# Optimization experiments

Hardware: AMD Instinct MI355X
Metric: run time of the kernel (lower is better)

Reference implementation:

```python
import jax, jax.numpy as jnp
import numpy as np

N_NODES = 100000
EMB_DIM = 64
N_EDGES = 1200000
N_LAYERS = 3


def setup_inputs() -> dict:
    key = jax.random.key(0)
    k1, k2, k3 = jax.random.split(key, 3)
    embedding = jax.random.normal(k1, (N_NODES, EMB_DIM), dtype=jnp.float32)
    layer_weights = jnp.ones((N_LAYERS + 1,), dtype=jnp.float32) / (N_LAYERS + 1)
    edge_weight = jax.random.uniform(k2, (N_EDGES,), dtype=jnp.float32)
    edge_index = jax.random.randint(k3, (2, N_EDGES), 0, N_NODES, dtype=jnp.int64)
    return {"embedding": embedding, "layer_weights": layer_weights,
            "edge_weight": edge_weight, "edge_index": edge_index}


def reference(embedding, layer_weights, edge_weight, edge_index):
    # LightGCN inference (dropout off). Each LGConv applies gcn_norm
    # (no self loops) then scatter-adds norm * x[src] into dst.
    n = embedding.shape[0]
    row, col = edge_index[0], edge_index[1]  # source, target

    # gcn_norm: deg over target nodes, symmetric normalization
    deg = jax.ops.segment_sum(edge_weight, col, num_segments=n)
    dinv = jnp.where(deg > 0, jax.lax.rsqrt(deg), 0.0)
    norm = dinv[row] * edge_weight * dinv[col]  # [E]

    x = embedding
    outs = [x]
    for _ in range(N_LAYERS):
        msgs = norm[:, None] * x[row]                         # [E, D] gather
        x = jax.ops.segment_sum(msgs, col, num_segments=n)    # [N, D] scatter
        outs.append(x)

    w = jax.nn.softmax(layer_weights)                         # [L+1]
    comb = jnp.einsum('l,lnd->nd', w, jnp.stack(outs))        # weighted layer combine
    # F.normalize(dim=1), eps=1e-12
    nrm = jnp.maximum(jnp.linalg.norm(comb, axis=1, keepdims=True), 1e-12)
    return comb / nrm
```

## Files before the change

kernel.cpp:

```cpp
#include <hip/hip_runtime.h>

#define N_NODES 100000
#define EMB_DIM 64
#define N_EDGES 1200000

#define BSHIFT  7
#define BNODES  128
#define NBUCKET ((N_NODES + BNODES - 1) / BNODES)
#define CAP     2048
#define EPB     4096
#define NBLK_BIN ((N_EDGES + EPB - 1) / EPB)

#define DBINS 512
#define DNPB  1024
#define NBLK_DEG ((N_NODES + DNPB - 1) / DNPB)

#define WSCALE 32767.0f
#define WINV   (1.0f / 32767.0f)

typedef unsigned short ushort8v __attribute__((ext_vector_type(8)));

struct __align__(8) BinRec {
    unsigned meta;
    float    ew;
};

__device__ __forceinline__ unsigned short f2bf(float f) {
    unsigned u = __float_as_uint(f);
    u += 0x7FFFu + ((u >> 16) & 1u);
    return (unsigned short)(u >> 16);
}
__device__ __forceinline__ float bf2f(unsigned short h) {
    return __uint_as_float((unsigned)h << 16);
}

__global__ void init_kernel(int* __restrict__ bucket_cursor, int* __restrict__ dhist) {
    int t = threadIdx.x;
    if (t < NBUCKET) bucket_cursor[t] = t * CAP;
    if (t < DBINS)   dhist[t] = 0;
}

__global__ void bin_scatter(const int* __restrict__ row,
                            const int* __restrict__ col,
                            const float* __restrict__ ew,
                            int* __restrict__ bucket_cursor,
                            BinRec* __restrict__ binned) {
    __shared__ int hcnt[NBUCKET];
    __shared__ int hbase[NBUCKET];
    int tid = threadIdx.x;
    if (tid < NBUCKET) hcnt[tid] = 0;
    __syncthreads();
    int base = blockIdx.x * EPB;
    int end = base + EPB; if (end > N_EDGES) end = N_EDGES;
    for (int e = base + tid; e < end; e += 1024)
        atomicAdd(&hcnt[col[e] >> BSHIFT], 1);
    __syncthreads();
    if (tid < NBUCKET) {
        int c = hcnt[tid];
        hbase[tid] = c ? atomicAdd(&bucket_cursor[tid], c) : 0;
        hcnt[tid] = 0;
    }
    __syncthreads();
    for (int e = base + tid; e < end; e += 1024) {
        int c = col[e];
        int b = c >> BSHIFT;
        int rk = atomicAdd(&hcnt[b], 1);
        BinRec r;
        r.meta = (unsigned)row[e] | ((unsigned)(c & (BNODES - 1)) << 20);
        r.ew = ew[e];
        binned[hbase[b] + rk] = r;
    }
}

__global__ void bucket_scan(const int* __restrict__ cursor,
                            int* __restrict__ csr_base,
                            int* __restrict__ start) {
    __shared__ int ws[16];
    int t = threadIdx.x;
    int lane = t & 63, wid = t >> 6;
    int v = (t < NBUCKET) ? (cursor[t] - t * CAP) : 0;
    int inc = v;
    #pragma unroll
    for (int o = 1; o < 64; o <<= 1) {
        int u = __shfl_up(inc, o, 64);
        if (lane >= o) inc += u;
    }
    if (lane == 63) ws[wid] = inc;
    __syncthreads();
    int woff = 0;
    for (int w = 0; w < wid; ++w) woff += ws[w];
    if (t < NBUCKET) csr_base[t] = woff + inc - v;
    if (t == 0) start[N_NODES] = N_EDGES;
}

__global__ void bucket_build(const BinRec* __restrict__ binned,
                             const int* __restrict__ cursor,
                             const int* __restrict__ csr_base,
                             const float* __restrict__ emb,
                             float* __restrict__ dinv,
                             float* __restrict__ rdinv,
                             int* __restrict__ start,
                             unsigned* __restrict__ rec,
                             unsigned short* __restrict__ y0,
                             int* __restrict__ dhist) {
    __shared__ BinRec lbin[CAP];
    __shared__ int   cnt[BNODES];
    __shared__ float deg[BNODES];
    __shared__ int   cur[BNODES];
    __shared__ int   dh[DBINS];
    __shared__ int   wsum[2];
    int b = blockIdx.x;
    int tid = threadIdx.x;
    if (tid < BNODES) { cnt[tid] = 0; deg[tid] = 0.0f; }
    for (int i = tid; i < DBINS; i += 256) dh[i] = 0;
    __syncthreads();
    int s = b * CAP;
    int n = cursor[b] - s;
    for (int i = tid; i < n; i += 256) {
        BinRec r = binned[s + i];
        lbin[i] = r;
        int l = r.meta >> 20;
        atomicAdd(&cnt[l], 1);
        atomicAdd(&deg[l], r.ew);
    }
    __syncthreads();
    int lane = tid & 63, wid = tid >> 6;
    int v = (tid < BNODES) ? cnt[tid] : 0;
    int inc = v;
    #pragma unroll
    for (int o = 1; o < 64; o <<= 1) {
        int u = __shfl_up(inc, o, 64);
        if (lane >= o) inc += u;
    }
    if (tid < BNODES && lane == 63) wsum[wid] = inc;
    __syncthreads();
    if (tid < BNODES) {
        int excl = inc - v + ((wid == 1) ? wsum[0] : 0);
        int node = (b << BSHIFT) + tid;
        if (node < N_NODES) {
            int st = csr_base[b] + excl;
            start[node] = st;
            cur[tid] = st;
            float d = deg[tid];
            dinv[node]  = (d > 0.0f) ? rsqrtf(d) : 0.0f;
            rdinv[node] = (d > 0.0f) ? sqrtf(d)  : 0.0f;
            int dd = v; if (dd > DBINS - 1) dd = DBINS - 1;
            atomicAdd(&dh[dd], 1);
        } else {
            cur[tid] = 0;
        }
    }
    __syncthreads();
    for (int i = tid; i < n; i += 256) {
        BinRec r = lbin[i];
        int l = r.meta >> 20;
        int pos = atomicAdd(&cur[l], 1);
        unsigned wq = (unsigned)rintf(r.ew * WSCALE);
        rec[pos] = ((r.meta & 0xFFFFFu) << 15) | wq;
    }
    for (int i = tid; i < DBINS; i += 256)
        if (dh[i]) atomicAdd(&dhist[i], dh[i]);
    #pragma unroll
    for (int pass = 0; pass < 4; ++pass) {
        int g = (pass * 256 + tid) * 8;
        int l = g >> 6;
        int node = (b << BSHIFT) + l;
        if (node < N_NODES) {
            float d = deg[l];
            float dn = (d > 0.0f) ? rsqrtf(d) : 0.0f;
            size_t off = (((size_t)node) << 6) + (g & 63);
            float4 a = *(const float4*)(emb + off);
            float4 bb = *(const float4*)(emb + off + 4);
            uint4 o;
            o.x = (unsigned)f2bf(dn * a.x)  | ((unsigned)f2bf(dn * a.y)  << 16);
            o.y = (unsigned)f2bf(dn * a.z)  | ((unsigned)f2bf(dn * a.w)  << 16);
            o.z = (unsigned)f2bf(dn * bb.x) | ((unsigned)f2bf(dn * bb.y) << 16);
            o.w = (unsigned)f2bf(dn * bb.z) | ((unsigned)f2bf(dn * bb.w) << 16);
            *(uint4*)(y0 + off) = o;
        }
    }
}

__global__ void deg_scan(const int* __restrict__ dhist, int* __restrict__ dcursor) {
    __shared__ int ws[8];
    int t = threadIdx.x;
    int lane = t & 63, wid = t >> 6;
    int v = dhist[t];
    int inc = v;
    #pragma unroll
    for (int o = 1; o < 64; o <<= 1) {
        int u = __shfl_up(inc, o, 64);
        if (lane >= o) inc += u;
    }
    if (lane == 63) ws[wid] = inc;
    __syncthreads();
    int woff = 0;
    for (int w = 0; w < wid; ++w) woff += ws[w];
    dcursor[t] = woff + inc - v;
}

__global__ void deg_scatter(const int* __restrict__ start,
                            int* __restrict__ dcursor,
                            int* __restrict__ perm) {
    __shared__ int h[DBINS];
    __shared__ int hb[DBINS];
    int tid = threadIdx.x;
    for (int i = tid; i < DBINS; i += 256) h[i] = 0;
    __syncthreads();
    int base = blockIdx.x * DNPB;
    int end = base + DNPB; if (end > N_NODES) end = N_NODES;
    for (int n = base + tid; n < end; n += 256) {
        int d = start[n + 1] - start[n];
        if (d > DBINS - 1) d = DBINS - 1;
        atomicAdd(&h[d], 1);
    }
    __syncthreads();
    for (int i = tid; i < DBINS; i += 256) {
        int c = h[i];
        hb[i] = c ? atomicAdd(&dcursor[i], c) : 0;
        h[i] = 0;
    }
    __syncthreads();
    for (int n = base + tid; n < end; n += 256) {
        int d = start[n + 1] - start[n];
        if (d > DBINS - 1) d = DBINS - 1;
        int rk = atomicAdd(&h[d], 1);
        perm[hb[d] + rk] = n;
    }
}

__device__ __forceinline__ void gather4(const unsigned* __restrict__ rec, int j,
                                        const unsigned short* __restrict__ yin, int q,
                                        float& a0, float& a1, float& a2, float& a3,
                                        float& a4, float& a5, float& a6, float& a7) {
    unsigned v0 = rec[j], v1 = rec[j + 1], v2 = rec[j + 2], v3 = rec[j + 3];
    ushort8v h0 = *(const ushort8v*)(yin + (((size_t)(v0 >> 15)) << 6) + q);
    ushort8v h1 = *(const ushort8v*)(yin + (((size_t)(v1 >> 15)) << 6) + q);
    ushort8v h2 = *(const ushort8v*)(yin + (((size_t)(v2 >> 15)) << 6) + q);
    ushort8v h3 = *(const ushort8v*)(yin + (((size_t)(v3 >> 15)) << 6) + q);
    float w0 = (float)(v0 & 0x7FFFu) * WINV, w1 = (float)(v1 & 0x7FFFu) * WINV;
    float w2 = (float)(v2 & 0x7FFFu) * WINV, w3 = (float)(v3 & 0x7FFFu) * WINV;
    a0 += w0*bf2f(h0[0]) + w1*bf2f(h1[0]) + w2*bf2f(h2[0]) + w3*bf2f(h3[0]);
    a1 += w0*bf2f(h0[1]) + w1*bf2f(h1[1]) + w2*bf2f(h2[1]) + w3*bf2f(h3[1]);
    a2 += w0*bf2f(h0[2]) + w1*bf2f(h1[2]) + w2*bf2f(h2[2]) + w3*bf2f(h3[2]);
    a3 += w0*bf2f(h0[3]) + w1*bf2f(h1[3]) + w2*bf2f(h2[3]) + w3*bf2f(h3[3]);
    a4 += w0*bf2f(h0[4]) + w1*bf2f(h1[4]) + w2*bf2f(h2[4]) + w3*bf2f(h3[4]);
    a5 += w0*bf2f(h0[5]) + w1*bf2f(h1[5]) + w2*bf2f(h2[5]) + w3*bf2f(h3[5]);
    a6 += w0*bf2f(h0[6]) + w1*bf2f(h1[6]) + w2*bf2f(h2[6]) + w3*bf2f(h3[6]);
    a7 += w0*bf2f(h0[7]) + w1*bf2f(h1[7]) + w2*bf2f(h2[7]) + w3*bf2f(h3[7]);
}

__device__ __forceinline__ void gather1(const unsigned* __restrict__ rec, int j,
                                        const unsigned short* __restrict__ yin, int q,
                                        float& a0, float& a1, float& a2, float& a3,
                                        float& a4, float& a5, float& a6, float& a7) {
    unsigned v = rec[j];
    ushort8v h = *(const ushort8v*)(yin + (((size_t)(v >> 15)) << 6) + q);
    float w = (float)(v & 0x7FFFu) * WINV;
    a0 += w * bf2f(h[0]); a1 += w * bf2f(h[1]);
    a2 += w * bf2f(h[2]); a3 += w * bf2f(h[3]);
    a4 += w * bf2f(h[4]); a5 += w * bf2f(h[5]);
    a6 += w * bf2f(h[6]); a7 += w * bf2f(h[7]);
}

#define ACC8 a0, a1, a2, a3, a4, a5, a6, a7

#define MERGE_SUBS()                                         \
    a0 += __shfl_xor(a0, 8, 64); a1 += __shfl_xor(a1, 8, 64); \
    a2 += __shfl_xor(a2, 8, 64); a3 += __shfl_xor(a3, 8, 64); \
    a4 += __shfl_xor(a4, 8, 64); a5 += __shfl_xor(a5, 8, 64); \
    a6 += __shfl_xor(a6, 8, 64); a7 += __shfl_xor(a7, 8, 64);

__global__ void prop8s_kernel(const unsigned short* __restrict__ yin,
                              unsigned short* __restrict__ yout,
                              const unsigned* __restrict__ rec,
                              const int* __restrict__ start,
                              const float* __restrict__ dinv,
                              const int* __restrict__ perm) {
    int t = blockIdx.x * blockDim.x + threadIdx.x;
    int g = t >> 4;
    int lane16 = t & 15;
    int sub = lane16 >> 3;
    int q = (lane16 & 7) << 3;
    if (g >= N_NODES) return;
    int n = perm[g];
    int s = start[n], e = start[n + 1];
    int d = e - s;
    int half = (d + 1) >> 1;
    int j  = s + sub * half;
    int j1 = sub ? e : s + half;

    float a0 = 0.f, a1 = 0.f, a2 = 0.f, a3 = 0.f;
    float a4 = 0.f, a5 = 0.f, a6 = 0.f, a7 = 0.f;
    for (; j + 4 <= j1; j += 4) gather4(rec, j, yin, q, ACC8);
    for (; j < j1; ++j)         gather1(rec, j, yin, q, ACC8);

    MERGE_SUBS();

    if (sub == 0) {
        float dn = dinv[n];
        float dn2 = dn * dn;
        uint4 o;
        o.x = (unsigned)f2bf(dn2 * a0) | ((unsigned)f2bf(dn2 * a1) << 16);
        o.y = (unsigned)f2bf(dn2 * a2) | ((unsigned)f2bf(dn2 * a3) << 16);
        o.z = (unsigned)f2bf(dn2 * a4) | ((unsigned)f2bf(dn2 * a5) << 16);
        o.w = (unsigned)f2bf(dn2 * a6) | ((unsigned)f2bf(dn2 * a7) << 16);
        *(uint4*)(yout + (((size_t)n) << 6) + q) = o;
    }
}

__global__ void prop8s_combine_kernel(const unsigned short* __restrict__ yin,
                                      const unsigned short* __restrict__ y0h,
                                      const unsigned short* __restrict__ y1h,
                                      const float* __restrict__ emb,
                                      const unsigned* __restrict__ rec,
                                      const int* __restrict__ start,
                                      const float* __restrict__ dinv,
                                      const float* __restrict__ rdinv,
                                      const float* __restrict__ lw,
                                      const int* __restrict__ perm,
                                      float* __restrict__ out) {
    int t = blockIdx.x * blockDim.x + threadIdx.x;
    int g = t >> 4;
    int lane16 = t & 15;
    int sub = lane16 >> 3;
    int q = (lane16 & 7) << 3;
    if (g >= N_NODES) return;
    int n = perm[g];
    int s = start[n], e = start[n + 1];
    int d = e - s;
    int half = (d + 1) >> 1;
    int j  = s + sub * half;
    int j1 = sub ? e : s + half;

    float a0 = 0.f, a1 = 0.f, a2 = 0.f, a3 = 0.f;
    float a4 = 0.f, a5 = 0.f, a6 = 0.f, a7 = 0.f;
    for (; j + 4 <= j1; j += 4) gather4(rec, j, yin, q, ACC8);
    for (; j < j1; ++j)         gather1(rec, j, yin, q, ACC8);

    MERGE_SUBS();

    if (sub == 0) {
        float dn = dinv[n];
        float rn = rdinv[n];

        float w0 = lw[0], w1 = lw[1], w2 = lw[2], w3 = lw[3];
        float m = fmaxf(fmaxf(w0, w1), fmaxf(w2, w3));
        float e0 = expf(w0 - m), e1 = expf(w1 - m), e2 = expf(w2 - m), e3 = expf(w3 - m);
        float inv_s = 1.0f / (e0 + e1 + e2 + e3);
        float c0 = e0 * rn, c1 = e1 * rn, c2 = e2 * rn, c3 = e3 * dn;

        size_t off = (((size_t)n) << 6) + q;
        float v0, v1, v2, v3, v4, v5, v6, v7;
        if (rn != 0.0f) {
            ushort8v h0v = *(const ushort8v*)(y0h + off);
            ushort8v h1v = *(const ushort8v*)(y1h + off);
            ushort8v h2v = *(const ushort8v*)(yin + off);
            v0 = (c0 * bf2f(h0v[0]) + c1 * bf2f(h1v[0]) + c2 * bf2f(h2v[0]) + c3 * a0) * inv_s;
            v1 = (c0 * bf2f(h0v[1]) + c1 * bf2f(h1v[1]) + c2 * bf2f(h2v[1]) + c3 * a1) * inv_s;
            v2 = (c0 * bf2f(h0v[2]) + c1 * bf2f(h1v[2]) + c2 * bf2f(h2v[2]) + c3 * a2) * inv_s;
            v3 = (c0 * bf2f(h0v[3]) + c1 * bf2f(h1v[3]) + c2 * bf2f(h2v[3]) + c3 * a3) * inv_s;
            v4 = (c0 * bf2f(h0v[4]) + c1 * bf2f(h1v[4]) + c2 * bf2f(h2v[4]) + c3 * a4) * inv_s;
            v5 = (c0 * bf2f(h0v[5]) + c1 * bf2f(h1v[5]) + c2 * bf2f(h2v[5]) + c3 * a5) * inv_s;
            v6 = (c0 * bf2f(h0v[6]) + c1 * bf2f(h1v[6]) + c2 * bf2f(h2v[6]) + c3 * a6) * inv_s;
            v7 = (c0 * bf2f(h0v[7]) + c1 * bf2f(h1v[7]) + c2 * bf2f(h2v[7]) + c3 * a7) * inv_s;
        } else {
            float4 xa = *(const float4*)(emb + off);
            float4 xb = *(const float4*)(emb + off + 4);
            float c = e0 * inv_s;
            v0 = c * xa.x; v1 = c * xa.y; v2 = c * xa.z; v3 = c * xa.w;
            v4 = c * xb.x; v5 = c * xb.y; v6 = c * xb.z; v7 = c * xb.w;
        }

        float sq = v0*v0 + v1*v1 + v2*v2 + v3*v3 + v4*v4 + v5*v5 + v6*v6 + v7*v7;
        #pragma unroll
        for (int o = 1; o < 8; o <<= 1) sq += __shfl_xor(sq, o, 64);
        float nrm = fmaxf(sqrtf(sq), 1e-12f);
        float inv_n = 1.0f / nrm;

        float4 oa, ob;
        oa.x = v0 * inv_n; oa.y = v1 * inv_n; oa.z = v2 * inv_n; oa.w = v3 * inv_n;
        ob.x = v4 * inv_n; ob.y = v5 * inv_n; ob.z = v6 * inv_n; ob.w = v7 * inv_n;
        *(float4*)(out + off) = oa;
        *(float4*)(out + off + 4) = ob;
    }
}

extern "C" void kernel_launch(void* const* d_in, const int* in_sizes, int n_in,
                              void* d_out, int out_size, void* d_ws, size_t ws_size,
                              hipStream_t stream) {
    const float* emb = (const float*)d_in[0];
    const float* lw  = (const float*)d_in[1];
    const float* ew  = (const float*)d_in[2];
    const int*   ei  = (const int*)d_in[3];
    const int* row = ei;
    const int* col = ei + N_EDGES;
    float* out = (float*)d_out;

    char* p = (char*)d_ws;
    BinRec*  binned = (BinRec*)p;               p += (size_t)NBUCKET * CAP * sizeof(BinRec);
    unsigned* rec   = (unsigned*)p;             p += (size_t)N_EDGES * 4;
    unsigned short* y0h = (unsigned short*)p;   p += (size_t)N_NODES * EMB_DIM * 2;
    unsigned short* y1h = (unsigned short*)p;   p += (size_t)N_NODES * EMB_DIM * 2;
    unsigned short* y2h = (unsigned short*)p;   p += (size_t)N_NODES * EMB_DIM * 2;
    float* dinv  = (float*)p;                   p += (size_t)N_NODES * 4;
    float* rdinv = (float*)p;                   p += (size_t)N_NODES * 4;
    int*   startA= (int*)p;                     p += (size_t)(N_NODES + 8) * 4;
    int*   perm  = (int*)p;                     p += (size_t)N_NODES * 4;
    int*   csr_base      = (int*)p;             p += (size_t)NBUCKET * 4;
    int*   bucket_cursor = (int*)p;             p += (size_t)NBUCKET * 4;
    int*   dhist   = (int*)p;                   p += (size_t)DBINS * 4;
    int*   dcursor = (int*)p;                   p += (size_t)DBINS * 4;

    const int B = 256;

    init_kernel<<<1, 1024, 0, stream>>>(bucket_cursor, dhist);
    bin_scatter<<<NBLK_BIN, 1024, 0, stream>>>(row, col, ew, bucket_cursor, binned);
    bucket_scan<<<1, 1024, 0, stream>>>(bucket_cursor, csr_base, startA);
    bucket_build<<<NBUCKET, B, 0, stream>>>(binned, bucket_cursor, csr_base, emb,
                                            dinv, rdinv, startA, rec, y0h, dhist);
    deg_scan<<<1, DBINS, 0, stream>>>(dhist, dcursor);
    deg_scatter<<<NBLK_DEG, B, 0, stream>>>(startA, dcursor, perm);

    long pt = (long)N_NODES * 16;
    int pgrid = (int)((pt + B - 1) / B);
    prop8s_kernel<<<pgrid, B, 0, stream>>>(y0h, y1h, rec, startA, dinv, perm);
    prop8s_kernel<<<pgrid, B, 0, stream>>>(y1h, y2h, rec, startA, dinv, perm);
    prop8s_combine_kernel<<<pgrid, B, 0, stream>>>(y2h, y0h, y1h, emb, rec, startA,
                                                   dinv, rdinv, lw, perm, out);
}
```

Before: 152.4 us.

## Use 8 lanes per node with prefetched edge records and reversed degree order

The propagation kernels now give each node 8 threads instead of 16, so the two-way edge split and the shuffle merge go away. The gather loop loads the next four edge records in software before the current ones are processed. Nodes are visited in reverse degree-sorted order, so high-degree nodes start first. bin_scatter also stages column indices in shared memory so they are not re-read from global memory. The trade-off is half the parallelism per node, which lengthens the serial chains for high-degree nodes, plus extra shared memory use in the binning kernel.

```diff
diff --git a/kernel.cpp b/kernel.cpp
--- a/kernel.cpp
+++ b/kernel.cpp
@@ -45,6 +45,7 @@
                             const float* __restrict__ ew,
                             int* __restrict__ bucket_cursor,
                             BinRec* __restrict__ binned) {
+    __shared__ int lcol[EPB];
     __shared__ int hcnt[NBUCKET];
     __shared__ int hbase[NBUCKET];
     int tid = threadIdx.x;
@@ -52,8 +53,11 @@
     __syncthreads();
     int base = blockIdx.x * EPB;
     int end = base + EPB; if (end > N_EDGES) end = N_EDGES;
-    for (int e = base + tid; e < end; e += 1024)
-        atomicAdd(&hcnt[col[e] >> BSHIFT], 1);
+    for (int e = base + tid; e < end; e += 1024) {
+        int c = col[e];
+        lcol[e - base] = c;
+        atomicAdd(&hcnt[c >> BSHIFT], 1);
+    }
     __syncthreads();
     if (tid < NBUCKET) {
         int c = hcnt[tid];
@@ -62,7 +66,7 @@
     }
     __syncthreads();
     for (int e = base + tid; e < end; e += 1024) {
-        int c = col[e];
+        int c = lcol[e - base];
         int b = c >> BSHIFT;
         int rk = atomicAdd(&hcnt[b], 1);
         BinRec r;
@@ -229,11 +233,10 @@
     }
 }
 
-__device__ __forceinline__ void gather4(const unsigned* __restrict__ rec, int j,
-                                        const unsigned short* __restrict__ yin, int q,
-                                        float& a0, float& a1, float& a2, float& a3,
-                                        float& a4, float& a5, float& a6, float& a7) {
-    unsigned v0 = rec[j], v1 = rec[j + 1], v2 = rec[j + 2], v3 = rec[j + 3];
+__device__ __forceinline__ void yfma4(unsigned v0, unsigned v1, unsigned v2, unsigned v3,
+                                      const unsigned short* __restrict__ yin, int q,
+                                      float& a0, float& a1, float& a2, float& a3,
+                                      float& a4, float& a5, float& a6, float& a7) {
     ushort8v h0 = *(const ushort8v*)(yin + (((size_t)(v0 >> 15)) << 6) + q);
     ushort8v h1 = *(const ushort8v*)(yin + (((size_t)(v1 >> 15)) << 6) + q);
     ushort8v h2 = *(const ushort8v*)(yin + (((size_t)(v2 >> 15)) << 6) + q);
@@ -250,11 +253,10 @@
     a7 += w0*bf2f(h0[7]) + w1*bf2f(h1[7]) + w2*bf2f(h2[7]) + w3*bf2f(h3[7]);
 }
 
-__device__ __forceinline__ void gather1(const unsigned* __restrict__ rec, int j,
-                                        const unsigned short* __restrict__ yin, int q,
-                                        float& a0, float& a1, float& a2, float& a3,
-                                        float& a4, float& a5, float& a6, float& a7) {
-    unsigned v = rec[j];
+__device__ __forceinline__ void yfma1(unsigned v,
+                                      const unsigned short* __restrict__ yin, int q,
+                                      float& a0, float& a1, float& a2, float& a3,
+                                      float& a4, float& a5, float& a6, float& a7) {
     ushort8v h = *(const ushort8v*)(yin + (((size_t)(v >> 15)) << 6) + q);
     float w = (float)(v & 0x7FFFu) * WINV;
     a0 += w * bf2f(h[0]); a1 += w * bf2f(h[1]);
@@ -265,125 +267,114 @@
 
 #define ACC8 a0, a1, a2, a3, a4, a5, a6, a7
 
-#define MERGE_SUBS()                                         \
-    a0 += __shfl_xor(a0, 8, 64); a1 += __shfl_xor(a1, 8, 64); \
-    a2 += __shfl_xor(a2, 8, 64); a3 += __shfl_xor(a3, 8, 64); \
-    a4 += __shfl_xor(a4, 8, 64); a5 += __shfl_xor(a5, 8, 64); \
-    a6 += __shfl_xor(a6, 8, 64); a7 += __shfl_xor(a7, 8, 64);
-
-__global__ void prop8s_kernel(const unsigned short* __restrict__ yin,
-                              unsigned short* __restrict__ yout,
-                              const unsigned* __restrict__ rec,
-                              const int* __restrict__ start,
-                              const float* __restrict__ dinv,
-                              const int* __restrict__ perm) {
+#define GATHER_BODY(yin)                                                        \
+    int j = s;                                                                  \
+    int rem = e - s;                                                            \
+    if (rem >= 8) {                                                             \
+        unsigned v0 = rec[j], v1 = rec[j+1], v2 = rec[j+2], v3 = rec[j+3];      \
+        while (rem >= 8) {                                                      \
+            unsigned n0 = rec[j+4], n1 = rec[j+5], n2 = rec[j+6], n3 = rec[j+7];\
+            yfma4(v0, v1, v2, v3, yin, q, ACC8);                                \
+            v0 = n0; v1 = n1; v2 = n2; v3 = n3;                                 \
+            j += 4; rem -= 4;                                                   \
+        }                                                                       \
+        yfma4(v0, v1, v2, v3, yin, q, ACC8);                                    \
+        j += 4; rem -= 4;                                                       \
+    } else if (rem >= 4) {                                                      \
+        unsigned v0 = rec[j], v1 = rec[j+1], v2 = rec[j+2], v3 = rec[j+3];      \
+        yfma4(v0, v1, v2, v3, yin, q, ACC8);                                    \
+        j += 4; rem -= 4;                                                       \
+    }                                                                           \
+    for (; rem > 0; --rem, ++j) yfma1(rec[j], yin, q, ACC8);
+
+__global__ void prop8_kernel(const unsigned short* __restrict__ yin,
+                             unsigned short* __restrict__ yout,
+                             const unsigned* __restrict__ rec,
+                             const int* __restrict__ start,
+                             const float* __restrict__ dinv,
+                             const int* __restrict__ perm) {
     int t = blockIdx.x * blockDim.x + threadIdx.x;
-    int g = t >> 4;
-    int lane16 = t & 15;
-    int sub = lane16 >> 3;
-    int q = (lane16 & 7) << 3;
-    if (g >= N_NODES) return;
-    int n = perm[g];
+    int slot = t >> 3;
+    int q = (t & 7) << 3;
+    if (slot >= N_NODES) return;
+    int n = perm[(N_NODES - 1) - slot];
     int s = start[n], e = start[n + 1];
-    int d = e - s;
-    int half = (d + 1) >> 1;
-    int j  = s + sub * half;
-    int j1 = sub ? e : s + half;
-
     float a0 = 0.f, a1 = 0.f, a2 = 0.f, a3 = 0.f;
     float a4 = 0.f, a5 = 0.f, a6 = 0.f, a7 = 0.f;
-    for (; j + 4 <= j1; j += 4) gather4(rec, j, yin, q, ACC8);
-    for (; j < j1; ++j)         gather1(rec, j, yin, q, ACC8);
-
-    MERGE_SUBS();
-
-    if (sub == 0) {
-        float dn = dinv[n];
-        float dn2 = dn * dn;
-        uint4 o;
-        o.x = (unsigned)f2bf(dn2 * a0) | ((unsigned)f2bf(dn2 * a1) << 16);
-        o.y = (unsigned)f2bf(dn2 * a2) | ((unsigned)f2bf(dn2 * a3) << 16);
-        o.z = (unsigned)f2bf(dn2 * a4) | ((unsigned)f2bf(dn2 * a5) << 16);
-        o.w = (unsigned)f2bf(dn2 * a6) | ((unsigned)f2bf(dn2 * a7) << 16);
-        *(uint4*)(yout + (((size_t)n) << 6) + q) = o;
-    }
-}
-
-__global__ void prop8s_combine_kernel(const unsigned short* __restrict__ yin,
-                                      const unsigned short* __restrict__ y0h,
-                                      const unsigned short* __restrict__ y1h,
-                                      const float* __restrict__ emb,
-                                      const unsigned* __restrict__ rec,
-                                      const int* __restrict__ start,
-                                      const float* __restrict__ dinv,
-                                      const float* __restrict__ rdinv,
-                                      const float* __restrict__ lw,
-                                      const int* __restrict__ perm,
-                                      float* __restrict__ out) {
+    GATHER_BODY(yin);
+    float dn = dinv[n];
+    float dn2 = dn * dn;
+    uint4 o;
+    o.x = (unsigned)f2bf(dn2 * a0) | ((unsigned)f2bf(dn2 * a1) << 16);
+    o.y = (unsigned)f2bf(dn2 * a2) | ((unsigned)f2bf(dn2 * a3) << 16);
+    o.z = (unsigned)f2bf(dn2 * a4) | ((unsigned)f2bf(dn2 * a5) << 16);
+    o.w = (unsigned)f2bf(dn2 * a6) | ((unsigned)f2bf(dn2 * a7) << 16);
+    *(uint4*)(yout + (((size_t)n) << 6) + q) = o;
+}
+
+__global__ void prop8_combine_kernel(const unsigned short* __restrict__ yin,
+                                     const unsigned short* __restrict__ y0h,
+                                     const unsigned short* __restrict__ y1h,
+                                     const float* __restrict__ emb,
+                                     const unsigned* __restrict__ rec,
+                                     const int* __restrict__ start,
+                                     const float* __restrict__ dinv,
+                                     const float* __restrict__ rdinv,
+                                     const float* __restrict__ lw,
+                                     const int* __restrict__ perm,
+                                     float* __restrict__ out) {
     int t = blockIdx.x * blockDim.x + threadIdx.x;
-    int g = t >> 4;
-    int lane16 = t & 15;
-    int sub = lane16 >> 3;
-    int q = (lane16 & 7) << 3;
-    if (g >= N_NODES) return;
-    int n = perm[g];
+    int slot = t >> 3;
+    int q = (t & 7) << 3;
+    if (slot >= N_NODES) return;
+    int n = perm[(N_NODES - 1) - slot];
     int s = start[n], e = start[n + 1];
-    int d = e - s;
-    int half = (d + 1) >> 1;
-    int j  = s + sub * half;
-    int j1 = sub ? e : s + half;
-
     float a0 = 0.f, a1 = 0.f, a2 = 0.f, a3 = 0.f;
     float a4 = 0.f, a5 = 0.f, a6 = 0.f, a7 = 0.f;
-    for (; j + 4 <= j1; j += 4) gather4(rec, j, yin, q, ACC8);
-    for (; j < j1; ++j)         gather1(rec, j, yin, q, ACC8);
-
-    MERGE_SUBS();
-
-    if (sub == 0) {
-        float dn = dinv[n];
-        float rn = rdinv[n];
-
-        float w0 = lw[0], w1 = lw[1], w2 = lw[2], w3 = lw[3];
-        float m = fmaxf(fmaxf(w0, w1), fmaxf(w2, w3));
-        float e0 = expf(w0 - m), e1 = expf(w1 - m), e2 = expf(w2 - m), e3 = expf(w3 - m);
-        float inv_s = 1.0f / (e0 + e1 + e2 + e3);
-        float c0 = e0 * rn, c1 = e1 * rn, c2 = e2 * rn, c3 = e3 * dn;
-
-        size_t off = (((size_t)n) << 6) + q;
-        float v0, v1, v2, v3, v4, v5, v6, v7;
-        if (rn != 0.0f) {
-            ushort8v h0v = *(const ushort8v*)(y0h + off);
-            ushort8v h1v = *(const ushort8v*)(y1h + off);
-            ushort8v h2v = *(const ushort8v*)(yin + off);
-            v0 = (c0 * bf2f(h0v[0]) + c1 * bf2f(h1v[0]) + c2 * bf2f(h2v[0]) + c3 * a0) * inv_s;
-            v1 = (c0 * bf2f(h0v[1]) + c1 * bf2f(h1v[1]) + c2 * bf2f(h2v[1]) + c3 * a1) * inv_s;
-            v2 = (c0 * bf2f(h0v[2]) + c1 * bf2f(h1v[2]) + c2 * bf2f(h2v[2]) + c3 * a2) * inv_s;
-            v3 = (c0 * bf2f(h0v[3]) + c1 * bf2f(h1v[3]) + c2 * bf2f(h2v[3]) + c3 * a3) * inv_s;
-            v4 = (c0 * bf2f(h0v[4]) + c1 * bf2f(h1v[4]) + c2 * bf2f(h2v[4]) + c3 * a4) * inv_s;
-            v5 = (c0 * bf2f(h0v[5]) + c1 * bf2f(h1v[5]) + c2 * bf2f(h2v[5]) + c3 * a5) * inv_s;
-            v6 = (c0 * bf2f(h0v[6]) + c1 * bf2f(h1v[6]) + c2 * bf2f(h2v[6]) + c3 * a6) * inv_s;
-            v7 = (c0 * bf2f(h0v[7]) + c1 * bf2f(h1v[7]) + c2 * bf2f(h2v[7]) + c3 * a7) * inv_s;
-        } else {
-            float4 xa = *(const float4*)(emb + off);
-            float4 xb = *(const float4*)(emb + off + 4);
-            float c = e0 * inv_s;
-            v0 = c * xa.x; v1 = c * xa.y; v2 = c * xa.z; v3 = c * xa.w;
-            v4 = c * xb.x; v5 = c * xb.y; v6 = c * xb.z; v7 = c * xb.w;
-        }
-
-        float sq = v0*v0 + v1*v1 + v2*v2 + v3*v3 + v4*v4 + v5*v5 + v6*v6 + v7*v7;
-        #pragma unroll
-        for (int o = 1; o < 8; o <<= 1) sq += __shfl_xor(sq, o, 64);
-        float nrm = fmaxf(sqrtf(sq), 1e-12f);
-        float inv_n = 1.0f / nrm;
-
-        float4 oa, ob;
-        oa.x = v0 * inv_n; oa.y = v1 * inv_n; oa.z = v2 * inv_n; oa.w = v3 * inv_n;
-        ob.x = v4 * inv_n; ob.y = v5 * inv_n; ob.z = v6 * inv_n; ob.w = v7 * inv_n;
-        *(float4*)(out + off) = oa;
-        *(float4*)(out + off + 4) = ob;
-    }
+    GATHER_BODY(yin);
+
+    float dn = dinv[n];
+    float rn = rdinv[n];
+
+    float w0 = lw[0], w1 = lw[1], w2 = lw[2], w3 = lw[3];
+    float m = fmaxf(fmaxf(w0, w1), fmaxf(w2, w3));
+    float e0 = expf(w0 - m), e1 = expf(w1 - m), e2 = expf(w2 - m), e3 = expf(w3 - m);
+    float inv_s = 1.0f / (e0 + e1 + e2 + e3);
+    float c0 = e0 * rn, c1 = e1 * rn, c2 = e2 * rn, c3 = e3 * dn;
+
+    size_t off = (((size_t)n) << 6) + q;
+    float v0, v1, v2, v3, v4, v5, v6, v7;
+    if (rn != 0.0f) {
+        ushort8v h0v = *(const ushort8v*)(y0h + off);
+        ushort8v h1v = *(const ushort8v*)(y1h + off);
+        ushort8v h2v = *(const ushort8v*)(yin + off);
+        v0 = (c0 * bf2f(h0v[0]) + c1 * bf2f(h1v[0]) + c2 * bf2f(h2v[0]) + c3 * a0) * inv_s;
+        v1 = (c0 * bf2f(h0v[1]) + c1 * bf2f(h1v[1]) + c2 * bf2f(h2v[1]) + c3 * a1) * inv_s;
+        v2 = (c0 * bf2f(h0v[2]) + c1 * bf2f(h1v[2]) + c2 * bf2f(h2v[2]) + c3 * a2) * inv_s;
+        v3 = (c0 * bf2f(h0v[3]) + c1 * bf2f(h1v[3]) + c2 * bf2f(h2v[3]) + c3 * a3) * inv_s;
+        v4 = (c0 * bf2f(h0v[4]) + c1 * bf2f(h1v[4]) + c2 * bf2f(h2v[4]) + c3 * a4) * inv_s;
+        v5 = (c0 * bf2f(h0v[5]) + c1 * bf2f(h1v[5]) + c2 * bf2f(h2v[5]) + c3 * a5) * inv_s;
+        v6 = (c0 * bf2f(h0v[6]) + c1 * bf2f(h1v[6]) + c2 * bf2f(h2v[6]) + c3 * a6) * inv_s;
+        v7 = (c0 * bf2f(h0v[7]) + c1 * bf2f(h1v[7]) + c2 * bf2f(h2v[7]) + c3 * a7) * inv_s;
+    } else {
+        float4 xa = *(const float4*)(emb + off);
+        float4 xb = *(const float4*)(emb + off + 4);
+        float c = e0 * inv_s;
+        v0 = c * xa.x; v1 = c * xa.y; v2 = c * xa.z; v3 = c * xa.w;
+        v4 = c * xb.x; v5 = c * xb.y; v6 = c * xb.z; v7 = c * xb.w;
+    }
+
+    float sq = v0*v0 + v1*v1 + v2*v2 + v3*v3 + v4*v4 + v5*v5 + v6*v6 + v7*v7;
+    #pragma unroll
+    for (int o = 1; o < 8; o <<= 1) sq += __shfl_xor(sq, o, 64);
+    float nrm = fmaxf(sqrtf(sq), 1e-12f);
+    float inv_n = 1.0f / nrm;
+
+    float4 oa, ob;
+    oa.x = v0 * inv_n; oa.y = v1 * inv_n; oa.z = v2 * inv_n; oa.w = v3 * inv_n;
+    ob.x = v4 * inv_n; ob.y = v5 * inv_n; ob.z = v6 * inv_n; ob.w = v7 * inv_n;
+    *(float4*)(out + off) = oa;
+    *(float4*)(out + off + 4) = ob;
 }
 
 extern "C" void kernel_launch(void* const* d_in, const int* in_sizes, int n_in,
@@ -422,10 +413,10 @@
     deg_scan<<<1, DBINS, 0, stream>>>(dhist, dcursor);
     deg_scatter<<<NBLK_DEG, B, 0, stream>>>(startA, dcursor, perm);
 
-    long pt = (long)N_NODES * 16;
+    long pt = (long)N_NODES * 8;
     int pgrid = (int)((pt + B - 1) / B);
-    prop8s_kernel<<<pgrid, B, 0, stream>>>(y0h, y1h, rec, startA, dinv, perm);
-    prop8s_kernel<<<pgrid, B, 0, stream>>>(y1h, y2h, rec, startA, dinv, perm);
-    prop8s_combine_kernel<<<pgrid, B, 0, stream>>>(y2h, y0h, y1h, emb, rec, startA,
-                                                   dinv, rdinv, lw, perm, out);
-}
+    prop8_kernel<<<pgrid, B, 0, stream>>>(y0h, y1h, rec, startA, dinv, perm);
+    prop8_kernel<<<pgrid, B, 0, stream>>>(y1h, y2h, rec, startA, dinv, perm);
+    prop8_combine_kernel<<<pgrid, B, 0, stream>>>(y2h, y0h, y1h, emb, rec, startA,
+                                                  dinv, rdinv, lw, perm, out);
+}
```

New measurement: 146.7 us. 1.04x faster.
